# Optimization experiments

Measured on AMD Instinct MI355X. Metric: run time of the kernel, lower is better.

## Reference

```python
import jax, jax.numpy as jnp
import numpy as np

B, D, O, E, K = 8192, 2048, 2048, 8, 2


def setup_inputs() -> dict:
    key = jax.random.key(0)
    k1, k2, k3, k4 = jax.random.split(key, 4)
    x = jax.random.normal(k1, (B, D), dtype=jnp.float32)
    # router: Linear(D -> E)
    router_w = jax.random.normal(k2, (E, D), dtype=jnp.float32) * (1.0 / np.sqrt(D))
    router_b = jnp.zeros((E,), dtype=jnp.float32)
    # experts: [E, O, D] weight (xavier-uniform-like scale), [E, O] bias (zeros)
    lim = np.sqrt(6.0 / (D + O))
    expert_w = jax.random.uniform(k3, (E, O, D), dtype=jnp.float32, minval=-lim, maxval=lim)
    expert_b = jnp.zeros((E, O), dtype=jnp.float32)
    return {"x": x, "router_w": router_w, "router_b": router_b,
            "expert_w": expert_w, "expert_b": expert_b}


def reference(x, router_w, router_b, expert_w, expert_b):
    # router logits [B, E]
    logits = x @ router_w.T + router_b
    top_vals, top_idx = jax.lax.top_k(logits, K)          # [B, K]
    routing_weights = jax.nn.softmax(top_vals, axis=-1)   # softmax over top-k logits
    # dense per-(token, expert) combine weight [B, E]; zero for unselected experts
    onehot = jax.nn.one_hot(top_idx, E, dtype=x.dtype)    # [B, K, E]
    w_be = jnp.einsum('bk,bke->be', routing_weights, onehot)
    # per-expert linear, weighted combine (loop over small fixed E)
    out = jnp.zeros((x.shape[0], O), dtype=x.dtype)
    for e in range(E):
        out = out + w_be[:, e:e + 1] * (x @ expert_w[e].T + expert_b[e])
    return out
```

## Files before the change

kernel.cpp:

```cpp
#include <hip/hip_runtime.h>
#include <stdint.h>

#define NB 8192
#define ND 2048
#define NO 2048
#define NE 8
#define BK 64
#define NT (ND / BK)
#define BM 256
#define BN 256
#define MAXW 72

typedef __bf16 bf16x8 __attribute__((ext_vector_type(8)));
typedef float floatx4 __attribute__((ext_vector_type(4)));

__device__ __forceinline__ unsigned short f2bf(float f) {
    union { float f; uint32_t u; } v; v.f = f;
    uint32_t u = v.u;
    return (unsigned short)((u + 0x7FFFu + ((u >> 16) & 1u)) >> 16);
}

__global__ __launch_bounds__(256) void cvt_zero_kernel(
        const float* __restrict__ w, unsigned short* __restrict__ ob,
        float* __restrict__ out) {
    const int n4W = NE * NO * ND / 4;
    const int n4O = NB * NO / 4;
    int i = blockIdx.x * blockDim.x + threadIdx.x;
    int stride = gridDim.x * blockDim.x;
    for (; i < n4W + n4O; i += stride) {
        if (i < n4W) {
            float4 v = ((const float4*)w)[i];
            ushort4 o;
            o.x = f2bf(v.x); o.y = f2bf(v.y); o.z = f2bf(v.z); o.w = f2bf(v.w);
            ((ushort4*)ob)[i] = o;
        } else {
            float4 z = {0.f, 0.f, 0.f, 0.f};
            ((float4*)out)[i - n4W] = z;
        }
    }
}

__global__ __launch_bounds__(256) void router_topk_kernel(const float* __restrict__ x,
        const float* __restrict__ rw, const float* __restrict__ rb,
        unsigned short* __restrict__ xbf,
        int* __restrict__ i0a, int* __restrict__ i1a,
        float* __restrict__ w0a, float* __restrict__ w1a,
        int* __restrict__ cnt) {
    if (blockIdx.x == 0 && threadIdx.x < NE) cnt[threadIdx.x] = 0;
    const int wave = threadIdx.x >> 6;
    const int lane = threadIdx.x & 63;
    const int t = blockIdx.x * 4 + wave;
    const float4* xp = (const float4*)(x + (size_t)t * ND);
    const float4* rp = (const float4*)rw;
    ushort4* xo = (ushort4*)(xbf + (size_t)t * ND);
    float acc[NE];
#pragma unroll
    for (int e = 0; e < NE; e++) acc[e] = 0.f;
#pragma unroll
    for (int i = 0; i < ND / 256; i++) {
        int idx = i * 64 + lane;
        float4 xv = xp[idx];
        ushort4 o;
        o.x = f2bf(xv.x); o.y = f2bf(xv.y); o.z = f2bf(xv.z); o.w = f2bf(xv.w);
        xo[idx] = o;
#pragma unroll
        for (int e = 0; e < NE; e++) {
            float4 rv = rp[(size_t)e * (ND / 4) + idx];
            acc[e] += xv.x * rv.x + xv.y * rv.y + xv.z * rv.z + xv.w * rv.w;
        }
    }
#pragma unroll
    for (int e = 0; e < NE; e++) {
        float v = acc[e];
#pragma unroll
        for (int s = 32; s > 0; s >>= 1) v += __shfl_xor(v, s, 64);
        acc[e] = v;
    }
    if (lane == 0) {
        float lg[NE];
#pragma unroll
        for (int e = 0; e < NE; e++) lg[e] = acc[e] + rb[e];
        int i0 = 0; float v0 = lg[0];
#pragma unroll
        for (int e = 1; e < NE; e++) if (lg[e] > v0) { v0 = lg[e]; i0 = e; }
        int i1 = -1; float v1 = -3.4e38f;
#pragma unroll
        for (int e = 0; e < NE; e++) if (e != i0 && lg[e] > v1) { v1 = lg[e]; i1 = e; }
        float ex = expf(v1 - v0);
        float inv = 1.f / (1.f + ex);
        i0a[t] = i0; i1a[t] = i1;
        w0a[t] = inv; w1a[t] = ex * inv;
    }
}

__global__ __launch_bounds__(256) void compact_kernel(
        const int* __restrict__ i0a, const int* __restrict__ i1a,
        const float* __restrict__ w0a, const float* __restrict__ w1a,
        int* __restrict__ cnt, int* __restrict__ tok, float* __restrict__ wl) {
    const int lane = threadIdx.x & 63;
    const int gw = (blockIdx.x * 256 + threadIdx.x) >> 6;
    const int t = gw * 64 + lane;
#pragma unroll
    for (int which = 0; which < 2; which++) {
        int sel   = which ? i1a[t] : i0a[t];
        float w   = which ? w1a[t] : w0a[t];
        unsigned long long m[NE];
#pragma unroll
        for (int e = 0; e < NE; e++) m[e] = __ballot(sel == e);
        int slot = __popcll(m[sel] & ((1ull << lane) - 1ull));
        int base = 0;
        if (lane < NE) base = atomicAdd(&cnt[lane], (int)__popcll(m[lane]));
        base = __shfl(base, sel, 64);
        tok[sel * NB + base + slot] = t;
        wl[sel * NB + base + slot]  = w;
    }
}

#define GLL16(g, l) __builtin_amdgcn_global_load_lds( \
    (const __attribute__((address_space(1))) void*)(g), \
    (__attribute__((address_space(3))) void*)(l), 16, 0, 0)

#define BAR __builtin_amdgcn_s_barrier()
#define WAITL asm volatile("s_waitcnt lgkmcnt(0)" ::: "memory")

#define LDA(HALFPTR) do {                                                   \
    const char* _p = (const char*)(HALFPTR);                                \
    _Pragma("unroll") for (int mi = 0; mi < 4; mi++)                        \
        _Pragma("unroll") for (int kk = 0; kk < 2; kk++)                    \
            af[mi][kk] = *(const bf16x8*)(_p + offA[mi][kk]);               \
} while (0)

#define LDB(HALFPTR) do {                                                   \
    const char* _p = (const char*)(HALFPTR);                                \
    _Pragma("unroll") for (int nj = 0; nj < 2; nj++)                        \
        _Pragma("unroll") for (int kk = 0; kk < 2; kk++)                    \
            bfr[nj][kk] = *(const bf16x8*)(_p + offB[nj][kk]);              \
} while (0)

#define MMAC(MH, NH) do {                                                   \
    __builtin_amdgcn_s_setprio(1);                                          \
    _Pragma("unroll") for (int kk = 0; kk < 2; kk++)                        \
        _Pragma("unroll") for (int mi = 0; mi < 4; mi++)                    \
            _Pragma("unroll") for (int nj = 0; nj < 2; nj++)                \
                acc[(MH)*4+mi][(NH)*2+nj] =                                 \
                    __builtin_amdgcn_mfma_f32_16x16x32_bf16(                \
                        af[mi][kk], bfr[nj][kk],                            \
                        acc[(MH)*4+mi][(NH)*2+nj], 0, 0, 0);                \
    __builtin_amdgcn_s_setprio(0);                                          \
} while (0)

#define STG_A(D, H, KT) do { if ((KT) < NT) {                               \
    GLL16(bA[H][0] + (size_t)(KT) * 128, (char*)sA[D][H] + tid * 16);       \
    GLL16(bA[H][1] + (size_t)(KT) * 128, (char*)sA[D][H] + 8192 + tid * 16);\
} } while (0)
#define STG_B(D, H, KT) do { if ((KT) < NT) {                               \
    GLL16(bB[H][0] + (size_t)(KT) * 128, (char*)sB[D][H] + tid * 16);       \
    GLL16(bB[H][1] + (size_t)(KT) * 128, (char*)sB[D][H] + 8192 + tid * 16);\
} } while (0)

__global__ __launch_bounds__(512, 2) void moe_gemm_kernel(
        const unsigned short* __restrict__ xbf, const unsigned short* __restrict__ wbf,
        const float* __restrict__ eb, const int* __restrict__ cntArr,
        const int* __restrict__ listTok, const float* __restrict__ listW,
        float* __restrict__ out) {
    __shared__ unsigned short sA[2][2][128 * 64];
    __shared__ unsigned short sB[2][2][128 * 64];

    const int bid = blockIdx.x;
    const int nt = bid & 7;
    const int widx = bid >> 3;
    int e = 0, mt = 0;
    {
        int acc0 = 0; int found = 0;
#pragma unroll
        for (int k = 0; k < NE; k++) {
            int nmt = (cntArr[k] + BM - 1) >> 8;
            if (!found && widx < acc0 + nmt) { e = k; mt = widx - acc0; found = 1; }
            acc0 += nmt;
        }
        if (!found) return;
    }
    const int cnt = cntArr[e];
    const int tid = threadIdx.x;

    const int prow0 = tid >> 3;
    const int prow1 = 64 + (tid >> 3);
    const int scol  = ((tid & 7) * 16) ^ (((tid >> 3) & 7) << 4);
    const char* bA[2][2]; const char* bB[2][2];
#pragma unroll
    for (int h = 0; h < 2; h++) {
        int g0 = mt * BM + h * 128 + prow0;
        int g1 = mt * BM + h * 128 + prow1;
        int tk0 = (g0 < cnt) ? listTok[e * NB + g0] : 0;
        int tk1 = (g1 < cnt) ? listTok[e * NB + g1] : 0;
        bA[h][0] = (const char*)xbf + (size_t)tk0 * (ND * 2) + scol;
        bA[h][1] = (const char*)xbf + (size_t)tk1 * (ND * 2) + scol;
        bB[h][0] = (const char*)wbf + ((size_t)e * NO + (size_t)nt * BN + h * 128 + prow0) * (ND * 2) + scol;
        bB[h][1] = (const char*)wbf + ((size_t)e * NO + (size_t)nt * BN + h * 128 + prow1) * (ND * 2) + scol;
    }

    const int wave = tid >> 6, lane = tid & 63;
    const int wm2 = wave >> 2;
    const int wn2 = wave & 3;
    const int lr = lane & 15, lq = lane >> 4;
    const int xorv = (lr & 7) << 4;
    int offA[4][2], offB[2][2];
#pragma unroll
    for (int mi = 0; mi < 4; mi++)
#pragma unroll
        for (int kk = 0; kk < 2; kk++)
            offA[mi][kk] = (wm2 * 64 + mi * 16 + lr) * 128 + ((kk * 64 + lq * 16) ^ xorv);
#pragma unroll
    for (int nj = 0; nj < 2; nj++)
#pragma unroll
        for (int kk = 0; kk < 2; kk++)
            offB[nj][kk] = (wn2 * 32 + nj * 16 + lr) * 128 + ((kk * 64 + lq * 16) ^ xorv);

    bf16x8 af[4][2], bfr[2][2];
    floatx4 acc[8][4];
#pragma unroll
    for (int i = 0; i < 8; i++)
#pragma unroll
        for (int j = 0; j < 4; j++) acc[i][j] = (floatx4){0.f, 0.f, 0.f, 0.f};

    STG_A(0, 0, 0); STG_A(0, 1, 0); STG_B(0, 0, 0); STG_B(0, 1, 0);
    STG_A(1, 0, 1); STG_A(1, 1, 1); STG_B(1, 1, 1);
    asm volatile("s_waitcnt vmcnt(6)" ::: "memory");
    BAR;

#pragma unroll 1
    for (int i = 0; i < NT / 2; i++) {
        const int t1 = 2 * i + 1, t2 = 2 * i + 2, t3 = 2 * i + 3;
        LDA(sA[0][0]); LDB(sB[0][0]);
        STG_B(1, 0, t1);
        BAR; MMAC(0, 0); WAITL; BAR;
        LDB(sB[0][1]);
        STG_A(0, 0, t2);
        BAR; MMAC(0, 1); WAITL; BAR;
        LDA(sA[0][1]);
        STG_B(0, 1, t2);
        BAR; MMAC(1, 1); WAITL; BAR;
        LDB(sB[0][0]);
        STG_A(0, 1, t2);
        BAR; MMAC(1, 0); WAITL;
        if (t2 < NT) { asm volatile("s_waitcnt vmcnt(6)" ::: "memory"); }
        else         { asm volatile("s_waitcnt vmcnt(0)" ::: "memory"); }
        BAR;
        LDA(sA[1][0]); LDB(sB[1][0]);
        STG_B(0, 0, t2);
        BAR; MMAC(0, 0); WAITL; BAR;
        LDB(sB[1][1]);
        STG_A(1, 0, t3);
        BAR; MMAC(0, 1); WAITL; BAR;
        LDA(sA[1][1]);
        STG_B(1, 1, t3);
        BAR; MMAC(1, 1); WAITL; BAR;
        LDB(sB[1][0]);
        STG_A(1, 1, t3);
        BAR; MMAC(1, 0); WAITL;
        if (t3 < NT) { asm volatile("s_waitcnt vmcnt(6)" ::: "memory"); }
        else         { asm volatile("s_waitcnt vmcnt(0)" ::: "memory"); }
        BAR;
    }

    float ebv[4];
#pragma unroll
    for (int nh = 0; nh < 2; nh++)
#pragma unroll
        for (int nj = 0; nj < 2; nj++)
            ebv[nh * 2 + nj] = eb[(size_t)e * NO + nt * BN + nh * 128 + wn2 * 32 + nj * 16 + lr];
#pragma unroll
    for (int mh = 0; mh < 2; mh++)
#pragma unroll
    for (int mi = 0; mi < 4; mi++)
#pragma unroll
    for (int r = 0; r < 4; r++) {
        int gr = mt * BM + mh * 128 + wm2 * 64 + mi * 16 + lq * 4 + r;
        if (gr < cnt) {
            int tk   = listTok[e * NB + gr];
            float wg = listW[e * NB + gr];
            float* op = out + (size_t)tk * NO + nt * BN + lr;
#pragma unroll
            for (int nh = 0; nh < 2; nh++)
#pragma unroll
            for (int nj = 0; nj < 2; nj++)
                atomicAdd(op + nh * 128 + wn2 * 32 + nj * 16,
                          wg * (acc[mh * 4 + mi][nh * 2 + nj][r] + ebv[nh * 2 + nj]));
        }
    }
}

extern "C" void kernel_launch(void* const* d_in, const int* in_sizes, int n_in,
                              void* d_out, int out_size, void* d_ws, size_t ws_size,
                              hipStream_t stream) {
    const float* x        = (const float*)d_in[0];
    const float* router_w = (const float*)d_in[1];
    const float* router_b = (const float*)d_in[2];
    const float* expert_w = (const float*)d_in[3];
    const float* expert_b = (const float*)d_in[4];
    float* out = (float*)d_out;
    char* ws = (char*)d_ws;

    unsigned short* xbf = (unsigned short*)ws;
    unsigned short* wbf = (unsigned short*)(ws + 33554432);
    size_t o = 100663296;
    int*   tokL = (int*)(ws + o);   o += NE * NB * 4;
    float* wL   = (float*)(ws + o); o += NE * NB * 4;
    int*   i0a  = (int*)(ws + o);   o += NB * 4;
    int*   i1a  = (int*)(ws + o);   o += NB * 4;
    float* w0a  = (float*)(ws + o); o += NB * 4;
    float* w1a  = (float*)(ws + o); o += NB * 4;
    int*   cnt  = (int*)(ws + o);   o += 128;

    router_topk_kernel<<<NB / 4, 256, 0, stream>>>(x, router_w, router_b, xbf,
                                                   i0a, i1a, w0a, w1a, cnt);
    cvt_zero_kernel<<<2048, 256, 0, stream>>>(expert_w, wbf, out);
    compact_kernel<<<NB / 64 / 4, 256, 0, stream>>>(i0a, i1a, w0a, w1a, cnt, tokL, wL);
    moe_gemm_kernel<<<MAXW * 8, 512, 0, stream>>>(
        xbf, wbf, expert_b, cnt, tokL, wL, out);
}
```

Baseline: 561.6 us.

## Split top-1 and top-2 routing into two GEMM passes with plain stores

Routing lists are split by slot: top-1 assignments go to one list and top-2 to another. The first GEMM pass writes the output directly and the second adds onto it with a read-modify-write instead of atomics. This removes the pass that zeroes the output and the atomic adds. In exchange there are two GEMM launches, which serialize, each with a smaller grid bound that could strand tiles if one expert gets many tokens.

```diff
diff --git a/kernel.cpp b/kernel.cpp
--- a/kernel.cpp
+++ b/kernel.cpp
@@ -9,7 +9,7 @@
 #define NT (ND / BK)
 #define BM 256
 #define BN 256
-#define MAXW 72
+#define MAXW 40
 
 typedef __bf16 bf16x8 __attribute__((ext_vector_type(8)));
 typedef float floatx4 __attribute__((ext_vector_type(4)));
@@ -20,23 +20,16 @@
     return (unsigned short)((u + 0x7FFFu + ((u >> 16) & 1u)) >> 16);
 }
 
-__global__ __launch_bounds__(256) void cvt_zero_kernel(
-        const float* __restrict__ w, unsigned short* __restrict__ ob,
-        float* __restrict__ out) {
+__global__ __launch_bounds__(256) void cvt_kernel(
+        const float* __restrict__ w, unsigned short* __restrict__ ob) {
     const int n4W = NE * NO * ND / 4;
-    const int n4O = NB * NO / 4;
     int i = blockIdx.x * blockDim.x + threadIdx.x;
     int stride = gridDim.x * blockDim.x;
-    for (; i < n4W + n4O; i += stride) {
-        if (i < n4W) {
-            float4 v = ((const float4*)w)[i];
-            ushort4 o;
-            o.x = f2bf(v.x); o.y = f2bf(v.y); o.z = f2bf(v.z); o.w = f2bf(v.w);
-            ((ushort4*)ob)[i] = o;
-        } else {
-            float4 z = {0.f, 0.f, 0.f, 0.f};
-            ((float4*)out)[i - n4W] = z;
-        }
+    for (; i < n4W; i += stride) {
+        float4 v = ((const float4*)w)[i];
+        ushort4 o;
+        o.x = f2bf(v.x); o.y = f2bf(v.y); o.z = f2bf(v.z); o.w = f2bf(v.w);
+        ((ushort4*)ob)[i] = o;
     }
 }
 
@@ -46,7 +39,7 @@
         int* __restrict__ i0a, int* __restrict__ i1a,
         float* __restrict__ w0a, float* __restrict__ w1a,
         int* __restrict__ cnt) {
-    if (blockIdx.x == 0 && threadIdx.x < NE) cnt[threadIdx.x] = 0;
+    if (blockIdx.x == 0 && threadIdx.x < 2 * NE) cnt[threadIdx.x] = 0;
     const int wave = threadIdx.x >> 6;
     const int lane = threadIdx.x & 63;
     const int t = blockIdx.x * 4 + wave;
@@ -96,7 +89,9 @@
 __global__ __launch_bounds__(256) void compact_kernel(
         const int* __restrict__ i0a, const int* __restrict__ i1a,
         const float* __restrict__ w0a, const float* __restrict__ w1a,
-        int* __restrict__ cnt, int* __restrict__ tok, float* __restrict__ wl) {
+        int* __restrict__ cntA, int* __restrict__ cntB,
+        int* __restrict__ tokA, float* __restrict__ wA,
+        int* __restrict__ tokB, float* __restrict__ wB) {
     const int lane = threadIdx.x & 63;
     const int gw = (blockIdx.x * 256 + threadIdx.x) >> 6;
     const int t = gw * 64 + lane;
@@ -104,6 +99,9 @@
     for (int which = 0; which < 2; which++) {
         int sel   = which ? i1a[t] : i0a[t];
         float w   = which ? w1a[t] : w0a[t];
+        int* cnt  = which ? cntB : cntA;
+        int* tok  = which ? tokB : tokA;
+        float* wl = which ? wB : wA;
         unsigned long long m[NE];
 #pragma unroll
         for (int e = 0; e < NE; e++) m[e] = __ballot(sel == e);
@@ -158,6 +156,7 @@
     GLL16(bB[H][1] + (size_t)(KT) * 128, (char*)sB[D][H] + 8192 + tid * 16);\
 } } while (0)
 
+template <bool ACCUM>
 __global__ __launch_bounds__(512, 2) void moe_gemm_kernel(
         const unsigned short* __restrict__ xbf, const unsigned short* __restrict__ wbf,
         const float* __restrict__ eb, const int* __restrict__ cntArr,
@@ -283,9 +282,12 @@
 #pragma unroll
             for (int nh = 0; nh < 2; nh++)
 #pragma unroll
-            for (int nj = 0; nj < 2; nj++)
-                atomicAdd(op + nh * 128 + wn2 * 32 + nj * 16,
-                          wg * (acc[mh * 4 + mi][nh * 2 + nj][r] + ebv[nh * 2 + nj]));
+            for (int nj = 0; nj < 2; nj++) {
+                float* p = op + nh * 128 + wn2 * 32 + nj * 16;
+                float v = wg * (acc[mh * 4 + mi][nh * 2 + nj][r] + ebv[nh * 2 + nj]);
+                if (ACCUM) v += *p;
+                *p = v;
+            }
         }
     }
 }
@@ -304,18 +306,25 @@
     unsigned short* xbf = (unsigned short*)ws;
     unsigned short* wbf = (unsigned short*)(ws + 33554432);
     size_t o = 100663296;
-    int*   tokL = (int*)(ws + o);   o += NE * NB * 4;
-    float* wL   = (float*)(ws + o); o += NE * NB * 4;
+    int*   tokA = (int*)(ws + o);   o += NE * NB * 4;
+    float* wA   = (float*)(ws + o); o += NE * NB * 4;
+    int*   tokB = (int*)(ws + o);   o += NE * NB * 4;
+    float* wB   = (float*)(ws + o); o += NE * NB * 4;
     int*   i0a  = (int*)(ws + o);   o += NB * 4;
     int*   i1a  = (int*)(ws + o);   o += NB * 4;
     float* w0a  = (float*)(ws + o); o += NB * 4;
     float* w1a  = (float*)(ws + o); o += NB * 4;
     int*   cnt  = (int*)(ws + o);   o += 128;
+    int* cntA = cnt;
+    int* cntB = cnt + 8;
 
     router_topk_kernel<<<NB / 4, 256, 0, stream>>>(x, router_w, router_b, xbf,
                                                    i0a, i1a, w0a, w1a, cnt);
-    cvt_zero_kernel<<<2048, 256, 0, stream>>>(expert_w, wbf, out);
-    compact_kernel<<<NB / 64 / 4, 256, 0, stream>>>(i0a, i1a, w0a, w1a, cnt, tokL, wL);
-    moe_gemm_kernel<<<MAXW * 8, 512, 0, stream>>>(
-        xbf, wbf, expert_b, cnt, tokL, wL, out);
-}
+    cvt_kernel<<<2048, 256, 0, stream>>>(expert_w, wbf);
+    compact_kernel<<<NB / 64 / 4, 256, 0, stream>>>(i0a, i1a, w0a, w1a,
+                                                    cntA, cntB, tokA, wA, tokB, wB);
+    moe_gemm_kernel<false><<<MAXW * 8, 512, 0, stream>>>(
+        xbf, wbf, expert_b, cntA, tokA, wA, out);
+    moe_gemm_kernel<true><<<MAXW * 8, 512, 0, stream>>>(
+        xbf, wbf, expert_b, cntB, tokB, wB, out);
+}
```

New measurement: 553.2 us. No clear change (-1.5%).
